# Performance work log

Hardware: AMD Instinct MI355X
Metric: run time of the kernel (lower is better)

## Reference

```python
import jax, jax.numpy as jnp
import numpy as np

INF = 1000000.0
B, S, D, N, H = 2, 2048, 1024, 16, 64
T = 2 * S
NORM = 1.0 / np.sqrt(H)


def _rel_shift(x, k_len, shift=1):
    # x: [b, n, f, t] -> Transformer-XL relative shift -> [b, n, f, k_len]
    b, n, f, t = x.shape
    y = x.reshape(b, n, t, f)[:, :, shift:, :].reshape(b, n, f, t - shift)
    return y[:, :, :, :k_len]


def setup_inputs() -> dict:
    key = jax.random.key(0)
    ks = jax.random.split(key, 16)
    inp = {}
    inp['q'] = jax.random.normal(ks[0], (B, S, D), jnp.float32)
    inp['k'] = jax.random.normal(ks[1], (B, S, D), jnp.float32)
    inp['v'] = jax.random.normal(ks[2], (B, S, D), jnp.float32)
    inp['pos_enc'] = jax.random.normal(ks[3], (T, D), jnp.float32)
    seg_ids = jax.random.randint(ks[4], (B, S), 0, 2)
    inp['seg_mat'] = seg_ids[:, :, None] == seg_ids[:, None, :]  # [B,S,S] bool
    # causal mask: 1 where attention is forbidden (j > i)
    causal = (jnp.arange(S)[None, :] > jnp.arange(S)[:, None]).astype(jnp.float32)
    inp['attn_mask'] = jnp.broadcast_to(causal[None, None], (B, 1, S, S))
    std = np.sqrt(1.0 / (D + N * H))
    inp['qW'] = jax.random.normal(ks[5], (D, N, H), jnp.float32) * std
    inp['kW'] = jax.random.normal(ks[6], (D, N, H), jnp.float32) * std
    inp['kb'] = jnp.zeros((N, H), jnp.float32)
    inp['vW'] = jax.random.normal(ks[7], (D, N, H), jnp.float32) * std
    inp['vb'] = jnp.zeros((N, H), jnp.float32)
    inp['r_w_bias'] = jax.random.uniform(ks[8], (N, H), jnp.float32, 0.0, 0.1)
    inp['r_r_bias'] = jax.random.uniform(ks[9], (N, H), jnp.float32, 0.0, 0.1)
    inp['r_kernel'] = jax.random.uniform(ks[10], (D, N, H), jnp.float32, 0.0, 0.1)
    inp['r_s_bias'] = jax.random.uniform(ks[11], (N, H), jnp.float32, 0.0, 0.1)
    inp['seg_embed'] = jax.random.uniform(ks[12], (2, N, H), jnp.float32, 0.0, 0.1)
    inp['postW'] = jax.random.normal(ks[13], (N, H, D), jnp.float32) * std
    inp['postb'] = jnp.zeros((D,), jnp.float32)
    inp['ln_g'] = jnp.ones((D,), jnp.float32)
    inp['ln_b'] = jnp.zeros((D,), jnp.float32)
    return inp


def reference(q, k, v, pos_enc, seg_mat, attn_mask, qW, kW, kb, vW, vb,
              r_w_bias, r_r_bias, r_kernel, r_s_bias, seg_embed,
              postW, postb, ln_g, ln_b):
    # head projections
    q_head = jnp.einsum('bid,dnh->binh', q, qW) * NORM
    k_head = jnp.einsum('bjd,dnh->bjnh', k, kW) + kb
    v_head = jnp.einsum('bjd,dnh->bjnh', v, vW) + vb
    # content score (r_w_bias also scaled by normalizer)
    content = jnp.einsum('binh,bjnh->bnij', q_head + r_w_bias * NORM, k_head)
    # relative position bias (rel_shift branch, shift=1)
    q_r = q_head + r_r_bias * NORM
    r_head = jnp.einsum('td,dnh->tnh', pos_enc, r_kernel)
    bd = jnp.einsum('bfnh,tnh->bnft', q_r, r_head)  # [B,N,S,T]
    pos_bias = _rel_shift(bd, S, shift=1)           # [B,N,S,S]
    # segment bias
    sb = jnp.einsum('binh,snh->bnis', q_head + r_s_bias * NORM, seg_embed)
    diff, same = sb[..., 0:1], sb[..., 1:2]         # [B,N,S,1]
    seg_bias = jnp.where(seg_mat[:, None], same, diff)  # [B,N,S,S]
    # combine, mask, softmax
    score = content + pos_bias + seg_bias
    score = score.astype(jnp.float32) - INF * attn_mask
    dist = jax.nn.softmax(score, axis=-1)
    # attention output
    attn_vec = jnp.einsum('bnij,bjnh->binh', dist, v_head)
    attn_out = jnp.einsum('binh,nhd->bid', attn_vec, postW) + postb
    # residual + layer norm
    x = q + attn_out
    mu = jnp.mean(x, axis=-1, keepdims=True)
    var = jnp.var(x, axis=-1, keepdims=True)
    return (x - mu) * jax.lax.rsqrt(var + 1e-5) * ln_g + ln_b
```

## Files before the change

kernel.cpp:

```cpp
#include <hip/hip_runtime.h>
#include <hip/hip_bf16.h>

typedef __attribute__((ext_vector_type(8))) short bf16x8;
typedef __attribute__((ext_vector_type(4))) float f32x4;
typedef unsigned short ushort_t;

#define S_LEN 2048
#define DMODEL 1024
#define NORM_F 0.125f

__device__ __forceinline__ short f2b(float x) {
  union { float f; unsigned u; } c; c.f = x;
  unsigned r = (c.u + 0x7FFFu + ((c.u >> 16) & 1u)) >> 16;
  return (short)r;
}
__device__ __forceinline__ float b2f(ushort_t u) {
  union { unsigned u; float f; } c; c.u = ((unsigned)u) << 16; return c.f;
}
__device__ __forceinline__ unsigned cvtpk(float lo, float hi) {
  unsigned r;
  asm volatile("v_cvt_pk_bf16_f32 %0, %1, %2" : "=v"(r) : "v"(lo), "v"(hi));
  return r;
}

__global__ void seg_extract_kernel(const unsigned int* __restrict__ seg_raw,
                                   unsigned* __restrict__ segw) {
  __shared__ int bad_int, bad_flt;
  int tid = threadIdx.x;
  if (tid == 0) { bad_int = 0; bad_flt = 0; }
  __syncthreads();
  for (int i = tid; i < 2048; i += 256) {
    unsigned v = seg_raw[i];
    if (v > 1u) atomicOr(&bad_int, 1);
    if (v != 0u && v != 0x3F800000u) atomicOr(&bad_flt, 1);
  }
  __syncthreads();
  int mode = bad_int ? (bad_flt ? 2 : 1) : 0;
  const unsigned char* u8 = (const unsigned char*)seg_raw;
  int P = blockIdx.x * 256 + tid;
  int b = P >> 11, i = P & 2047;
  size_t off = (size_t)b * S_LEN * S_LEN + i;
  int bit;
  if (mode == 0)      bit = (int)(seg_raw[off] & 1u);
  else if (mode == 1) bit = (seg_raw[off] != 0u) ? 1 : 0;
  else                bit = (int)(u8[off] & 1u);
  unsigned long long mk = __ballot(bit);
  if ((tid & 63) == 0) {
    segw[P >> 5] = (unsigned)mk;
    segw[(P >> 5) + 1] = (unsigned)(mk >> 32);
  }
}

__global__ __launch_bounds__(256) void conv4_kernel(
    const float* __restrict__ s0, const float* __restrict__ s1,
    const float* __restrict__ s2, const float* __restrict__ s3,
    ushort_t* __restrict__ d0, ushort_t* __restrict__ d1,
    ushort_t* __restrict__ d2, ushort_t* __restrict__ d3) {
  int z = blockIdx.y;
  const float* src = z == 0 ? s0 : z == 1 ? s1 : z == 2 ? s2 : s3;
  ushort_t* dst = z == 0 ? d0 : z == 1 ? d1 : z == 2 ? d2 : d3;
  size_t base = ((size_t)blockIdx.x * 256 + threadIdx.x) * 8;
  float4 a = *(const float4*)(src + base);
  float4 b = *(const float4*)(src + base + 4);
  union { ushort_t us[8]; uint4 v; } o;
  o.us[0] = (ushort_t)f2b(a.x); o.us[1] = (ushort_t)f2b(a.y);
  o.us[2] = (ushort_t)f2b(a.z); o.us[3] = (ushort_t)f2b(a.w);
  o.us[4] = (ushort_t)f2b(b.x); o.us[5] = (ushort_t)f2b(b.y);
  o.us[6] = (ushort_t)f2b(b.z); o.us[7] = (ushort_t)f2b(b.w);
  *(uint4*)(dst + base) = o.v;
}

__global__ __launch_bounds__(256) void convT_kernel(
    const float* __restrict__ s0, const float* __restrict__ s1,
    const float* __restrict__ s2, const float* __restrict__ s3,
    const float* __restrict__ s4,
    ushort_t* __restrict__ d0, ushort_t* __restrict__ d1,
    ushort_t* __restrict__ d2, ushort_t* __restrict__ d3,
    ushort_t* __restrict__ d4) {
  int z = blockIdx.z;
  const float* src = z == 0 ? s0 : z == 1 ? s1 : z == 2 ? s2 : z == 3 ? s3 : s4;
  ushort_t* dst = z == 0 ? d0 : z == 1 ? d1 : z == 2 ? d2 : z == 3 ? d3 : d4;
  __shared__ float Tl[64][68];
  int tid = threadIdx.x;
  int k0 = blockIdx.x * 64, n0 = blockIdx.y * 64;
#pragma unroll
  for (int it = 0; it < 4; ++it) {
    int idx = tid + it * 256;
    int r = idx >> 4, c4 = (idx & 15) * 4;
    *(float4*)&Tl[r][c4] = *(const float4*)(src + (size_t)(k0 + r) * 1024 + n0 + c4);
  }
  __syncthreads();
#pragma unroll
  for (int it = 0; it < 2; ++it) {
    int idx = tid + it * 256;
    int nn = idx >> 3, kc = idx & 7;
    union { ushort_t us[8]; uint4 v; } o;
#pragma unroll
    for (int e = 0; e < 8; ++e) o.us[e] = (ushort_t)f2b(Tl[kc * 8 + e][nn]);
    *(uint4*)(dst + (size_t)(n0 + nn) * 1024 + k0 + kc * 8) = o.v;
  }
}

template <bool OUTBF>
__global__ __launch_bounds__(256) void gemm_bf_kernel(
    const ushort_t* __restrict__ A, const ushort_t* __restrict__ Wt,
    const float* __restrict__ bias, void* __restrict__ Cv, float scale) {
  __shared__ short A_lds[128][40];
  __shared__ short B_lds[128][40];
  const int tid = threadIdx.x;
  const int wave = tid >> 6, lane = tid & 63;
  const int r16 = lane & 15, g = lane >> 4;
  const int wm = wave >> 1, wn = wave & 1;
  const int m0 = blockIdx.x * 128, n0 = blockIdx.y * 128;
  const int sr = tid >> 2, sseg = (tid & 3) * 8;
  f32x4 acc[4][4] = {};
  uint4 ra0 = *(const uint4*)(A + (size_t)(m0 + sr) * 1024 + sseg);
  uint4 ra1 = *(const uint4*)(A + (size_t)(m0 + 64 + sr) * 1024 + sseg);
  uint4 rb0 = *(const uint4*)(Wt + (size_t)(n0 + sr) * 1024 + sseg);
  uint4 rb1 = *(const uint4*)(Wt + (size_t)(n0 + 64 + sr) * 1024 + sseg);
  for (int k0 = 0; k0 < 1024; k0 += 32) {
    *(uint4*)&A_lds[sr][sseg] = ra0;
    *(uint4*)&A_lds[64 + sr][sseg] = ra1;
    *(uint4*)&B_lds[sr][sseg] = rb0;
    *(uint4*)&B_lds[64 + sr][sseg] = rb1;
    __syncthreads();
    if (k0 + 32 < 1024) {
      ra0 = *(const uint4*)(A + (size_t)(m0 + sr) * 1024 + k0 + 32 + sseg);
      ra1 = *(const uint4*)(A + (size_t)(m0 + 64 + sr) * 1024 + k0 + 32 + sseg);
      rb0 = *(const uint4*)(Wt + (size_t)(n0 + sr) * 1024 + k0 + 32 + sseg);
      rb1 = *(const uint4*)(Wt + (size_t)(n0 + 64 + sr) * 1024 + k0 + 32 + sseg);
    }
    bf16x8 af[4], bfr[4];
#pragma unroll
    for (int fm = 0; fm < 4; ++fm)
      af[fm] = *(const bf16x8*)&A_lds[wm * 64 + fm * 16 + r16][g * 8];
#pragma unroll
    for (int fn = 0; fn < 4; ++fn)
      bfr[fn] = *(const bf16x8*)&B_lds[wn * 64 + fn * 16 + r16][g * 8];
#pragma unroll
    for (int fm = 0; fm < 4; ++fm)
#pragma unroll
      for (int fn = 0; fn < 4; ++fn)
        acc[fm][fn] = __builtin_amdgcn_mfma_f32_16x16x32_bf16(af[fm], bfr[fn], acc[fm][fn], 0, 0, 0);
    __syncthreads();
  }
  float bv[4];
#pragma unroll
  for (int fn = 0; fn < 4; ++fn)
    bv[fn] = bias ? bias[n0 + wn * 64 + fn * 16 + r16] : 0.f;
#pragma unroll
  for (int fm = 0; fm < 4; ++fm)
#pragma unroll
    for (int fn = 0; fn < 4; ++fn)
#pragma unroll
      for (int rr = 0; rr < 4; ++rr) {
        float vv = acc[fm][fn][rr] * scale + bv[fn];
        size_t off = (size_t)(m0 + wm * 64 + fm * 16 + g * 4 + rr) * 1024 +
                     n0 + wn * 64 + fn * 16 + r16;
        if (OUTBF) ((ushort_t*)Cv)[off] = (ushort_t)f2b(vv);
        else       ((float*)Cv)[off] = vv;
      }
}

__global__ __launch_bounds__(256) void gemm4_kernel(
    const ushort_t* __restrict__ a0, const ushort_t* __restrict__ a1,
    const ushort_t* __restrict__ a2, const ushort_t* __restrict__ a3,
    const ushort_t* __restrict__ w0, const ushort_t* __restrict__ w1,
    const ushort_t* __restrict__ w2, const ushort_t* __restrict__ w3,
    const float* __restrict__ kb, const float* __restrict__ vb,
    ushort_t* __restrict__ c0, ushort_t* __restrict__ c1,
    ushort_t* __restrict__ c2, ushort_t* __restrict__ c3) {
  const int z = blockIdx.z;
  const ushort_t* A  = z == 0 ? a0 : z == 1 ? a1 : z == 2 ? a2 : a3;
  const ushort_t* Wt = z == 0 ? w0 : z == 1 ? w1 : z == 2 ? w2 : w3;
  const float* bias  = z == 1 ? kb : z == 2 ? vb : (const float*)nullptr;
  ushort_t* C        = z == 0 ? c0 : z == 1 ? c1 : z == 2 ? c2 : c3;
  const float scale  = z == 0 ? NORM_F : 1.0f;

  __shared__ short A_lds[128][40];
  __shared__ short B_lds[128][40];
  const int tid = threadIdx.x;
  const int wave = tid >> 6, lane = tid & 63;
  const int r16 = lane & 15, g = lane >> 4;
  const int wm = wave >> 1, wn = wave & 1;
  const int m0 = blockIdx.x * 128, n0 = blockIdx.y * 128;
  const int sr = tid >> 2, sseg = (tid & 3) * 8;
  f32x4 acc[4][4] = {};
  uint4 ra0 = *(const uint4*)(A + (size_t)(m0 + sr) * 1024 + sseg);
  uint4 ra1 = *(const uint4*)(A + (size_t)(m0 + 64 + sr) * 1024 + sseg);
  uint4 rb0 = *(const uint4*)(Wt + (size_t)(n0 + sr) * 1024 + sseg);
  uint4 rb1 = *(const uint4*)(Wt + (size_t)(n0 + 64 + sr) * 1024 + sseg);
  for (int k0 = 0; k0 < 1024; k0 += 32) {
    *(uint4*)&A_lds[sr][sseg] = ra0;
    *(uint4*)&A_lds[64 + sr][sseg] = ra1;
    *(uint4*)&B_lds[sr][sseg] = rb0;
    *(uint4*)&B_lds[64 + sr][sseg] = rb1;
    __syncthreads();
    if (k0 + 32 < 1024) {
      ra0 = *(const uint4*)(A + (size_t)(m0 + sr) * 1024 + k0 + 32 + sseg);
      ra1 = *(const uint4*)(A + (size_t)(m0 + 64 + sr) * 1024 + k0 + 32 + sseg);
      rb0 = *(const uint4*)(Wt + (size_t)(n0 + sr) * 1024 + k0 + 32 + sseg);
      rb1 = *(const uint4*)(Wt + (size_t)(n0 + 64 + sr) * 1024 + k0 + 32 + sseg);
    }
    bf16x8 af[4], bfr[4];
#pragma unroll
    for (int fm = 0; fm < 4; ++fm)
      af[fm] = *(const bf16x8*)&A_lds[wm * 64 + fm * 16 + r16][g * 8];
#pragma unroll
    for (int fn = 0; fn < 4; ++fn)
      bfr[fn] = *(const bf16x8*)&B_lds[wn * 64 + fn * 16 + r16][g * 8];
#pragma unroll
    for (int fm = 0; fm < 4; ++fm)
#pragma unroll
      for (int fn = 0; fn < 4; ++fn)
        acc[fm][fn] = __builtin_amdgcn_mfma_f32_16x16x32_bf16(af[fm], bfr[fn], acc[fm][fn], 0, 0, 0);
    __syncthreads();
  }
  float bv[4];
#pragma unroll
  for (int fn = 0; fn < 4; ++fn)
    bv[fn] = bias ? bias[n0 + wn * 64 + fn * 16 + r16] : 0.f;
#pragma unroll
  for (int fm = 0; fm < 4; ++fm)
#pragma unroll
    for (int fn = 0; fn < 4; ++fn)
#pragma unroll
      for (int rr = 0; rr < 4; ++rr) {
        float vv = acc[fm][fn][rr] * scale + bv[fn];
        size_t off = (size_t)(m0 + wm * 64 + fm * 16 + g * 4 + rr) * 1024 +
                     n0 + wn * 64 + fn * 16 + r16;
        C[off] = (ushort_t)f2b(vv);
      }
}

__global__ __launch_bounds__(256) void qprep_kernel(
    const ushort_t* __restrict__ qh, const float* __restrict__ rwb,
    const float* __restrict__ rrb, const float* __restrict__ rsb,
    const float* __restrict__ sem, ushort_t* __restrict__ qwb,
    ushort_t* __restrict__ qrb, float2* __restrict__ sbp) {
  const int tid = threadIdx.x;
  const int w = tid >> 6, lane = tid & 63;
  const int c0 = lane * 16;
  float rwbN[16], rrbN[16], rsbN[16], s0v[16], s1v[16];
#pragma unroll
  for (int u = 0; u < 16; u += 4) {
    *(float4*)&rwbN[u] = *(const float4*)(rwb + c0 + u);
    *(float4*)&rrbN[u] = *(const float4*)(rrb + c0 + u);
    *(float4*)&rsbN[u] = *(const float4*)(rsb + c0 + u);
    *(float4*)&s0v[u]  = *(const float4*)(sem + c0 + u);
    *(float4*)&s1v[u]  = *(const float4*)(sem + 1024 + c0 + u);
  }
#pragma unroll
  for (int u = 0; u < 16; ++u) { rwbN[u] *= NORM_F; rrbN[u] *= NORM_F; rsbN[u] *= NORM_F; }
  for (int r = 0; r < 16; ++r) {
    int row = blockIdx.x * 64 + w * 16 + r;
    const ushort_t* qp = qh + (size_t)row * 1024 + c0;
    union { uint4 v; ushort_t us[8]; } qa, qb;
    qa.v = *(const uint4*)qp; qb.v = *(const uint4*)(qp + 8);
    float p0 = 0.f, p1 = 0.f;
    union { ushort_t us[8]; uint4 v; } w0, w1, r0, r1;
#pragma unroll
    for (int u = 0; u < 16; ++u) {
      float qv = b2f(u < 8 ? qa.us[u] : qb.us[u - 8]);
      ushort_t cw = (ushort_t)f2b(qv + rwbN[u]);
      ushort_t cr = (ushort_t)f2b(qv + rrbN[u]);
      if (u < 8) { w0.us[u] = cw; r0.us[u] = cr; }
      else       { w1.us[u - 8] = cw; r1.us[u - 8] = cr; }
      float qs = qv + rsbN[u];
      p0 += qs * s0v[u]; p1 += qs * s1v[u];
    }
    *(uint4*)(qwb + (size_t)row * 1024 + c0)     = w0.v;
    *(uint4*)(qwb + (size_t)row * 1024 + c0 + 8) = w1.v;
    *(uint4*)(qrb + (size_t)row * 1024 + c0)     = r0.v;
    *(uint4*)(qrb + (size_t)row * 1024 + c0 + 8) = r1.v;
    p0 += __shfl_xor(p0, 1); p0 += __shfl_xor(p0, 2);
    p1 += __shfl_xor(p1, 1); p1 += __shfl_xor(p1, 2);
    if ((lane & 3) == 0) {
      int bI = row >> 11, iI = row & 2047, nI = lane >> 2;
      sbp[((size_t)bI * 16 + nI) * 2048 + iI] = make_float2(p0, p1);
    }
  }
}

__global__ __launch_bounds__(256) void attn_kernel(
    const ushort_t* __restrict__ qwb, const ushort_t* __restrict__ qrb,
    const ushort_t* __restrict__ khb, const ushort_t* __restrict__ vhb,
    const ushort_t* __restrict__ rhb, const float2* __restrict__ sbp,
    const unsigned* __restrict__ segw, ushort_t* __restrict__ opart,
    float* __restrict__ ml) {
  __shared__ short Klds[64][64];
  __shared__ short Rlds[128][64];
  __shared__ short VsT[2][64][72];
  __shared__ short SP[4][1376];

  const int tid = threadIdx.x;
  const int w = tid >> 6, lane = tid & 63;
  const int r16 = lane & 15, g = lane >> 4;
  const int lin = (int)blockIdx.x;
  const int grp = (lin & 7) + ((lin >> 9) << 3);
  const int j = (lin >> 3) & 63;
  const int x = 31 - (j >> 1);
  const int hx = j & 1;
  const int i0 = x * 64;
  const int nh = (x + 2) >> 1;
  const int tbeg = hx ? nh : 0;
  const int tend = hx ? (x + 1) : nh;
  const int n = grp & 15, b = grp >> 4;
  const int BNS = 65536;
  const int rowbase = (b * 16 + n) * 2048 + i0;

  if (tbeg >= tend) {
    const int il0 = w * 16 + g * 4;
#pragma unroll
    for (int rr = 0; rr < 4; ++rr) {
#pragma unroll
      for (int s = 0; s < 4; ++s)
        opart[(size_t)(BNS + rowbase + il0 + rr) * 64 + s * 16 + r16] = 0;
      if (r16 == 0) {
        ml[2 * BNS + rowbase + il0 + rr] = -1e30f;
        ml[3 * BNS + rowbase + il0 + rr] = 0.f;
      }
    }
    return;
  }

  short* SPw = &SP[w][0];
  const int srow = tid >> 3, sg8 = (tid & 7) * 8;

  const int qrow = i0 + w * 16 + r16;
  const ushort_t* qwp = qwb + (size_t)(b * S_LEN + qrow) * DMODEL + n * 64 + g * 8;
  const ushort_t* qrp = qrb + (size_t)(b * S_LEN + qrow) * DMODEL + n * 64 + g * 8;
  bf16x8 qw[2], qr[2];
  qw[0] = *(const bf16x8*)qwp;  qw[1] = *(const bf16x8*)(qwp + 32);
  qr[0] = *(const bf16x8*)qrp;  qr[1] = *(const bf16x8*)(qrp + 32);
  float2 sbv = sbp[((size_t)b * 16 + n) * 2048 + qrow];
  const float sb0 = sbv.x, sb1 = sbv.y;
  const int ai = (segw[b * 64 + (qrow >> 5)] >> (qrow & 31)) & 1;
  const int iw0 = i0 + w * 16;

  {
    const int j0 = tbeg * 64;
    const int W0 = 2048 + j0 - i0 - 63;
#pragma unroll
    for (int it = 0; it < 2; ++it) {
      int qk = tid + it * 256, row = qk >> 3, cl = qk & 7;
      uint4 kv = *(const uint4*)(khb + (size_t)(b * S_LEN + j0 + row) * DMODEL + n * 64 + cl * 8);
      *(uint4*)&Klds[row][(cl ^ (row & 7)) * 8] = kv;
    }
#pragma unroll
    for (int it = 0; it < 4; ++it) {
      int qk = tid + it * 256, row = qk >> 3, cl = qk & 7;
      uint4 rv = *(const uint4*)(rhb + (size_t)(W0 + row) * DMODEL + n * 64 + cl * 8);
      *(uint4*)&Rlds[row][(cl ^ (row & 7)) * 8] = rv;
    }
#pragma unroll
    for (int it = 0; it < 2; ++it) {
      int jj = srow + it * 32;
      union { uint4 v; ushort_t us[8]; } vv;
      vv.v = *(const uint4*)(vhb + (size_t)(b * S_LEN + j0 + jj) * DMODEL + n * 64 + sg8);
#pragma unroll
      for (int e = 0; e < 8; ++e) {
        int hh = sg8 + e;
        VsT[0][hh][((jj >> 3) ^ ((hh >> 3) & 3)) * 8 + (jj & 7)] = (short)vv.us[e];
      }
    }
  }

  float m_r = -1e30f, l_r = 0.f;
  f32x4 o[4] = {};

  for (int t = tbeg; t < tend; ++t) {
    const int j0 = t * 64;
    const int tt = (t - tbeg) & 1;
    const bool hasn = (t + 1 < tend);
    __syncthreads();

    uint4 kpf[2], rpf[4], vpf[2];
    if (hasn) {
      const int j0n = j0 + 64;
      const int W0n = 2048 + j0n - i0 - 63;
#pragma unroll
      for (int it = 0; it < 2; ++it) {
        int qk = tid + it * 256, row = qk >> 3, cl = qk & 7;
        kpf[it] = *(const uint4*)(khb + (size_t)(b * S_LEN + j0n + row) * DMODEL + n * 64 + cl * 8);
      }
#pragma unroll
      for (int it = 0; it < 4; ++it) {
        int qk = tid + it * 256, row = qk >> 3, cl = qk & 7;
        rpf[it] = *(const uint4*)(rhb + (size_t)(W0n + row) * DMODEL + n * 64 + cl * 8);
      }
#pragma unroll
      for (int it = 0; it < 2; ++it)
        vpf[it] = *(const uint4*)(vhb + (size_t)(b * S_LEN + j0n + srow + it * 32) * DMODEL + n * 64 + sg8);
    }
    unsigned wlo = segw[b * 64 + (j0 >> 5)];
    unsigned whi = segw[b * 64 + (j0 >> 5) + 1];

    f32x4 cf[4] = {};
#pragma unroll
    for (int s = 0; s < 4; ++s) {
      int row = s * 16 + r16;
      bf16x8 k0 = *(const bf16x8*)&Klds[row][(g ^ (row & 7)) * 8];
      bf16x8 k1 = *(const bf16x8*)&Klds[row][((4 + g) ^ (row & 7)) * 8];
      cf[s] = __builtin_amdgcn_mfma_f32_16x16x32_bf16(k0, qw[0], cf[s], 0, 0, 0);
      cf[s] = __builtin_amdgcn_mfma_f32_16x16x32_bf16(k1, qw[1], cf[s], 0, 0, 0);
    }
#pragma unroll
    for (int sp = 0; sp < 5; ++sp) {
      int row = 48 - w * 16 + sp * 16 + r16;
      bf16x8 r0 = *(const bf16x8*)&Rlds[row][(g ^ (row & 7)) * 8];
      bf16x8 r1 = *(const bf16x8*)&Rlds[row][((4 + g) ^ (row & 7)) * 8];
      f32x4 pf = {};
      pf = __builtin_amdgcn_mfma_f32_16x16x32_bf16(r0, qr[0], pf, 0, 0, 0);
      pf = __builtin_amdgcn_mfma_f32_16x16x32_bf16(r1, qr[1], pf, 0, 0, 0);
      uint2 pw;
      pw.x = cvtpk(pf[0], pf[1]);
      pw.y = cvtpk(pf[2], pf[3]);
      *(uint2*)&SPw[r16 * 84 + sp * 16 + g * 4] = pw;
    }
    ushort_t pu[4][4];
#pragma unroll
    for (int s = 0; s < 4; ++s)
#pragma unroll
      for (int rr = 0; rr < 4; ++rr)
        pu[s][rr] = (ushort_t)SPw[r16 * 84 + (15 - r16) + s * 16 + g * 4 + rr];
    float vals[4][4];
    float vmax = -1e30f;
    const bool diag = (t == x);
#pragma unroll
    for (int s = 0; s < 4; ++s) {
      unsigned word = (s < 2) ? wlo : whi;
#pragma unroll
      for (int rr = 0; rr < 4; ++rr) {
        int p = s * 16 + g * 4 + rr;
        int bitv = (word >> (p & 31)) & 1;
        float sv = cf[s][rr] + b2f(pu[s][rr]) + ((bitv == ai) ? sb1 : sb0);
        if (diag && (p > w * 16 + r16)) sv -= 1e6f;
        vals[s][rr] = sv;
        vmax = fmaxf(vmax, sv);
      }
    }
    vmax = fmaxf(vmax, __shfl_xor(vmax, 16));
    vmax = fmaxf(vmax, __shfl_xor(vmax, 32));
    float scl = 1.f;
    bool resc = !__all(vmax <= m_r + 8.f);
    if (resc) {
      float mnew = fmaxf(m_r, vmax);
      scl = __expf(m_r - mnew);
      m_r = mnew;
    }
    float pex[4][4];
    float psum = 0.f;
#pragma unroll
    for (int s = 0; s < 4; ++s)
#pragma unroll
      for (int rr = 0; rr < 4; ++rr) {
        pex[s][rr] = __expf(vals[s][rr] - m_r);
        psum += pex[s][rr];
      }
    l_r = l_r * scl + psum;
#pragma unroll
    for (int s = 0; s < 4; ++s) {
      uint2 pw;
      pw.x = cvtpk(pex[s][0], pex[s][1]);
      pw.y = cvtpk(pex[s][2], pex[s][3]);
      *(uint2*)&SPw[r16 * 72 + s * 16 + g * 4] = pw;
    }
    __syncthreads();

    if (hasn) {
#pragma unroll
      for (int it = 0; it < 2; ++it) {
        int qk = tid + it * 256, row = qk >> 3, cl = qk & 7;
        *(uint4*)&Klds[row][(cl ^ (row & 7)) * 8] = kpf[it];
      }
#pragma unroll
      for (int it = 0; it < 4; ++it) {
        int qk = tid + it * 256, row = qk >> 3, cl = qk & 7;
        *(uint4*)&Rlds[row][(cl ^ (row & 7)) * 8] = rpf[it];
      }
      const int dst = tt ^ 1;
#pragma unroll
      for (int it = 0; it < 2; ++it) {
        int jj = srow + it * 32;
        union { uint4 v; ushort_t us[8]; } vv; vv.v = vpf[it];
#pragma unroll
        for (int e = 0; e < 8; ++e) {
          int hh = sg8 + e;
          VsT[dst][hh][((jj >> 3) ^ ((hh >> 3) & 3)) * 8 + (jj & 7)] = (short)vv.us[e];
        }
      }
    }
    if (resc) {
      float sclb[4];
#pragma unroll
      for (int rr = 0; rr < 4; ++rr) sclb[rr] = __shfl(scl, g * 4 + rr);
#pragma unroll
      for (int s = 0; s < 4; ++s)
#pragma unroll
        for (int rr = 0; rr < 4; ++rr) o[s][rr] *= sclb[rr];
    }
    bf16x8 pa0 = *(const bf16x8*)&SPw[r16 * 72 + g * 8];
    bf16x8 pa1 = *(const bf16x8*)&SPw[r16 * 72 + 32 + g * 8];
#pragma unroll
    for (int s = 0; s < 4; ++s) {
      int hh = s * 16 + r16;
      bf16x8 v0 = *(const bf16x8*)&VsT[tt][hh][(g ^ ((hh >> 3) & 3)) * 8];
      bf16x8 v1 = *(const bf16x8*)&VsT[tt][hh][((4 + g) ^ ((hh >> 3) & 3)) * 8];
      o[s] = __builtin_amdgcn_mfma_f32_16x16x32_bf16(pa0, v0, o[s], 0, 0, 0);
      o[s] = __builtin_amdgcn_mfma_f32_16x16x32_bf16(pa1, v1, o[s], 0, 0, 0);
    }
  }

  float l_row = l_r;
  l_row += __shfl_xor(l_row, 16);
  l_row += __shfl_xor(l_row, 32);
  if (lane < 16) {
    ml[hx * 2 * BNS + rowbase + w * 16 + r16] = m_r;
    ml[(hx * 2 + 1) * BNS + rowbase + w * 16 + r16] = l_row;
  }
#pragma unroll
  for (int s = 0; s < 4; ++s)
#pragma unroll
    for (int rr = 0; rr < 4; ++rr) {
      const int il = w * 16 + g * 4 + rr;
      opart[(size_t)(hx * BNS + rowbase + il) * 64 + s * 16 + r16] = (ushort_t)f2b(o[s][rr]);
    }
}

__global__ __launch_bounds__(256) void merge_kernel(
    const ushort_t* __restrict__ opart, const float* __restrict__ ml,
    ushort_t* __restrict__ av) {
  const int BNS = 65536;
  int row = blockIdx.x * 4 + (threadIdx.x >> 6);
  int lane = threadIdx.x & 63;
  float m0 = ml[row], l0 = ml[BNS + row];
  float m1 = ml[2 * BNS + row], l1 = ml[3 * BNS + row];
  float m = fmaxf(m0, m1);
  float a0 = __expf(m0 - m), a1 = __expf(m1 - m);
  float inv = 1.f / (l0 * a0 + l1 * a1);
  float o0 = b2f(opart[(size_t)row * 64 + lane]);
  float o1 = b2f(opart[(size_t)(BNS + row) * 64 + lane]);
  float ov = (o0 * a0 + o1 * a1) * inv;
  int bI = row >> 15, nI = (row >> 11) & 15, iI = row & 2047;
  av[(size_t)(bI * 2048 + iI) * 1024 + nI * 64 + lane] = (ushort_t)f2b(ov);
}

__global__ __launch_bounds__(256) void ln_kernel(
    const float* __restrict__ q, const float* __restrict__ ao,
    const float* __restrict__ ln_g, const float* __restrict__ ln_b,
    float* __restrict__ out) {
  int row = blockIdx.x;
  const float* xq = q + (size_t)row * 1024;
  const float* xa = ao + (size_t)row * 1024;
  float x[4], lsum = 0.f, lsq = 0.f;
#pragma unroll
  for (int e = 0; e < 4; ++e) {
    int d = threadIdx.x + e * 256;
    x[e] = xq[d] + xa[d];
    lsum += x[e]; lsq += x[e] * x[e];
  }
  for (int off = 1; off < 64; off <<= 1) {
    lsum += __shfl_xor(lsum, off);
    lsq += __shfl_xor(lsq, off);
  }
  __shared__ float red[8];
  int wv = threadIdx.x >> 6, ln = threadIdx.x & 63;
  if (ln == 0) { red[wv] = lsum; red[4 + wv] = lsq; }
  __syncthreads();
  lsum = red[0] + red[1] + red[2] + red[3];
  lsq = red[4] + red[5] + red[6] + red[7];
  float mu = lsum * (1.f / 1024.f);
  float var = lsq * (1.f / 1024.f) - mu * mu;
  float inv = rsqrtf(var + 1e-5f);
#pragma unroll
  for (int e = 0; e < 4; ++e) {
    int d = threadIdx.x + e * 256;
    out[(size_t)row * 1024 + d] = (x[e] - mu) * inv * ln_g[d] + ln_b[d];
  }
}

extern "C" void kernel_launch(void* const* d_in, const int* in_sizes, int n_in,
                              void* d_out, int out_size, void* d_ws, size_t ws_size,
                              hipStream_t stream) {
  const float* q   = (const float*)d_in[0];
  const float* k   = (const float*)d_in[1];
  const float* v   = (const float*)d_in[2];
  const float* pe  = (const float*)d_in[3];
  const void*  seg = d_in[4];
  const float* qW  = (const float*)d_in[6];
  const float* kW  = (const float*)d_in[7];
  const float* kb  = (const float*)d_in[8];
  const float* vW  = (const float*)d_in[9];
  const float* vb  = (const float*)d_in[10];
  const float* rwb = (const float*)d_in[11];
  const float* rrb = (const float*)d_in[12];
  const float* rK  = (const float*)d_in[13];
  const float* rsb = (const float*)d_in[14];
  const float* sem = (const float*)d_in[15];
  const float* pW  = (const float*)d_in[16];
  const float* pb  = (const float*)d_in[17];
  const float* lng = (const float*)d_in[18];
  const float* lnb = (const float*)d_in[19];
  float* out = (float*)d_out;

  const size_t MB = 1u << 20;
  char* W = (char*)d_ws;
  ushort_t* abq  = (ushort_t*)(W + 0 * MB);
  ushort_t* abk  = (ushort_t*)(W + 8 * MB);
  ushort_t* abv  = (ushort_t*)(W + 16 * MB);
  ushort_t* abpe = (ushort_t*)(W + 24 * MB);
  ushort_t* wtq  = (ushort_t*)(W + 32 * MB);
  ushort_t* wtk  = (ushort_t*)(W + 34 * MB);
  ushort_t* wtv  = (ushort_t*)(W + 36 * MB);
  ushort_t* wtr  = (ushort_t*)(W + 38 * MB);
  ushort_t* wtp  = (ushort_t*)(W + 40 * MB);
  ushort_t* qh   = (ushort_t*)(W + 42 * MB);
  ushort_t* kh   = (ushort_t*)(W + 50 * MB);
  ushort_t* vh   = (ushort_t*)(W + 58 * MB);
  ushort_t* rh   = (ushort_t*)(W + 66 * MB);
  unsigned* segw = (unsigned*)(W + 74 * MB);
  float2*   sbp  = (float2*)(W + 74 * MB + 65536);
  float*    ml   = (float*)(W + 75 * MB);
  ushort_t* qwb   = (ushort_t*)(W + 0 * MB);
  ushort_t* qrb   = (ushort_t*)(W + 8 * MB);
  ushort_t* opart = (ushort_t*)(W + 16 * MB);
  ushort_t* av    = (ushort_t*)(W + 42 * MB);
  float*    ao    = (float*)(W + 50 * MB);

  seg_extract_kernel<<<dim3(16), dim3(256), 0, stream>>>((const unsigned int*)seg, segw);
  conv4_kernel<<<dim3(2048, 4), dim3(256), 0, stream>>>(q, k, v, pe, abq, abk, abv, abpe);
  convT_kernel<<<dim3(16, 16, 5), dim3(256), 0, stream>>>(qW, kW, vW, rK, pW,
                                                          wtq, wtk, wtv, wtr, wtp);
  gemm4_kernel<<<dim3(32, 8, 4), dim3(256), 0, stream>>>(
      abq, abk, abv, abpe, wtq, wtk, wtv, wtr, kb, vb, qh, kh, vh, rh);

  qprep_kernel<<<dim3(64), dim3(256), 0, stream>>>(qh, rwb, rrb, rsb, sem, qwb, qrb, sbp);

  attn_kernel<<<dim3(2048), dim3(256), 0, stream>>>(qwb, qrb, kh, vh, rh,
                                                    sbp, segw, opart, ml);
  merge_kernel<<<dim3(16384), dim3(256), 0, stream>>>(opart, ml, av);

  gemm_bf_kernel<false><<<dim3(32, 8), dim3(256), 0, stream>>>(av, wtp, pb, ao, 1.0f);
  ln_kernel<<<dim3(4096), dim3(256), 0, stream>>>(q, ao, lng, lnb, out);
}
```

Before: 283.2 us.

## Retile post GEMM, split qprep blocks, widen V swizzle, add MFMA priority hints

The output projection GEMM now uses 64-row tiles, launching twice as many blocks to fill more CUs. qprep runs as 256 single-wave blocks instead of 64 four-wave blocks. The V-transpose LDS swizzle XORs the full hh>>3 to spread bank accesses more widely. s_setprio hints around the score and PV MFMA sections favour matrix issue across waves. Smaller tiles lower per-block data reuse, and the priority hints may do little.

```diff
diff --git a/kernel.cpp b/kernel.cpp
--- a/kernel.cpp
+++ b/kernel.cpp
@@ -101,10 +101,21 @@
   }
 }
 
-template <bool OUTBF>
-__global__ __launch_bounds__(256) void gemm_bf_kernel(
-    const ushort_t* __restrict__ A, const ushort_t* __restrict__ Wt,
-    const float* __restrict__ bias, void* __restrict__ Cv, float scale) {
+__global__ __launch_bounds__(256) void gemm4_kernel(
+    const ushort_t* __restrict__ a0, const ushort_t* __restrict__ a1,
+    const ushort_t* __restrict__ a2, const ushort_t* __restrict__ a3,
+    const ushort_t* __restrict__ w0, const ushort_t* __restrict__ w1,
+    const ushort_t* __restrict__ w2, const ushort_t* __restrict__ w3,
+    const float* __restrict__ kb, const float* __restrict__ vb,
+    ushort_t* __restrict__ c0, ushort_t* __restrict__ c1,
+    ushort_t* __restrict__ c2, ushort_t* __restrict__ c3) {
+  const int z = blockIdx.z;
+  const ushort_t* A  = z == 0 ? a0 : z == 1 ? a1 : z == 2 ? a2 : a3;
+  const ushort_t* Wt = z == 0 ? w0 : z == 1 ? w1 : z == 2 ? w2 : w3;
+  const float* bias  = z == 1 ? kb : z == 2 ? vb : (const float*)nullptr;
+  ushort_t* C        = z == 0 ? c0 : z == 1 ? c1 : z == 2 ? c2 : c3;
+  const float scale  = z == 0 ? NORM_F : 1.0f;
+
   __shared__ short A_lds[128][40];
   __shared__ short B_lds[128][40];
   const int tid = threadIdx.x;
@@ -157,60 +168,44 @@
         float vv = acc[fm][fn][rr] * scale + bv[fn];
         size_t off = (size_t)(m0 + wm * 64 + fm * 16 + g * 4 + rr) * 1024 +
                      n0 + wn * 64 + fn * 16 + r16;
-        if (OUTBF) ((ushort_t*)Cv)[off] = (ushort_t)f2b(vv);
-        else       ((float*)Cv)[off] = vv;
-      }
-}
-
-__global__ __launch_bounds__(256) void gemm4_kernel(
-    const ushort_t* __restrict__ a0, const ushort_t* __restrict__ a1,
-    const ushort_t* __restrict__ a2, const ushort_t* __restrict__ a3,
-    const ushort_t* __restrict__ w0, const ushort_t* __restrict__ w1,
-    const ushort_t* __restrict__ w2, const ushort_t* __restrict__ w3,
-    const float* __restrict__ kb, const float* __restrict__ vb,
-    ushort_t* __restrict__ c0, ushort_t* __restrict__ c1,
-    ushort_t* __restrict__ c2, ushort_t* __restrict__ c3) {
-  const int z = blockIdx.z;
-  const ushort_t* A  = z == 0 ? a0 : z == 1 ? a1 : z == 2 ? a2 : a3;
-  const ushort_t* Wt = z == 0 ? w0 : z == 1 ? w1 : z == 2 ? w2 : w3;
-  const float* bias  = z == 1 ? kb : z == 2 ? vb : (const float*)nullptr;
-  ushort_t* C        = z == 0 ? c0 : z == 1 ? c1 : z == 2 ? c2 : c3;
-  const float scale  = z == 0 ? NORM_F : 1.0f;
-
-  __shared__ short A_lds[128][40];
+        C[off] = (ushort_t)f2b(vv);
+      }
+}
+
+__global__ __launch_bounds__(256) void gemm_post_kernel(
+    const ushort_t* __restrict__ A, const ushort_t* __restrict__ Wt,
+    const float* __restrict__ bias, float* __restrict__ C) {
+  __shared__ short A_lds[64][40];
   __shared__ short B_lds[128][40];
   const int tid = threadIdx.x;
   const int wave = tid >> 6, lane = tid & 63;
   const int r16 = lane & 15, g = lane >> 4;
   const int wm = wave >> 1, wn = wave & 1;
-  const int m0 = blockIdx.x * 128, n0 = blockIdx.y * 128;
+  const int m0 = blockIdx.x * 64, n0 = blockIdx.y * 128;
   const int sr = tid >> 2, sseg = (tid & 3) * 8;
-  f32x4 acc[4][4] = {};
+  f32x4 acc[2][4] = {};
   uint4 ra0 = *(const uint4*)(A + (size_t)(m0 + sr) * 1024 + sseg);
-  uint4 ra1 = *(const uint4*)(A + (size_t)(m0 + 64 + sr) * 1024 + sseg);
   uint4 rb0 = *(const uint4*)(Wt + (size_t)(n0 + sr) * 1024 + sseg);
   uint4 rb1 = *(const uint4*)(Wt + (size_t)(n0 + 64 + sr) * 1024 + sseg);
   for (int k0 = 0; k0 < 1024; k0 += 32) {
     *(uint4*)&A_lds[sr][sseg] = ra0;
-    *(uint4*)&A_lds[64 + sr][sseg] = ra1;
     *(uint4*)&B_lds[sr][sseg] = rb0;
     *(uint4*)&B_lds[64 + sr][sseg] = rb1;
     __syncthreads();
     if (k0 + 32 < 1024) {
       ra0 = *(const uint4*)(A + (size_t)(m0 + sr) * 1024 + k0 + 32 + sseg);
-      ra1 = *(const uint4*)(A + (size_t)(m0 + 64 + sr) * 1024 + k0 + 32 + sseg);
       rb0 = *(const uint4*)(Wt + (size_t)(n0 + sr) * 1024 + k0 + 32 + sseg);
       rb1 = *(const uint4*)(Wt + (size_t)(n0 + 64 + sr) * 1024 + k0 + 32 + sseg);
     }
-    bf16x8 af[4], bfr[4];
-#pragma unroll
-    for (int fm = 0; fm < 4; ++fm)
-      af[fm] = *(const bf16x8*)&A_lds[wm * 64 + fm * 16 + r16][g * 8];
+    bf16x8 af[2], bfr[4];
+#pragma unroll
+    for (int fm = 0; fm < 2; ++fm)
+      af[fm] = *(const bf16x8*)&A_lds[wm * 32 + fm * 16 + r16][g * 8];
 #pragma unroll
     for (int fn = 0; fn < 4; ++fn)
       bfr[fn] = *(const bf16x8*)&B_lds[wn * 64 + fn * 16 + r16][g * 8];
 #pragma unroll
-    for (int fm = 0; fm < 4; ++fm)
+    for (int fm = 0; fm < 2; ++fm)
 #pragma unroll
       for (int fn = 0; fn < 4; ++fn)
         acc[fm][fn] = __builtin_amdgcn_mfma_f32_16x16x32_bf16(af[fm], bfr[fn], acc[fm][fn], 0, 0, 0);
@@ -221,25 +216,23 @@
   for (int fn = 0; fn < 4; ++fn)
     bv[fn] = bias ? bias[n0 + wn * 64 + fn * 16 + r16] : 0.f;
 #pragma unroll
-  for (int fm = 0; fm < 4; ++fm)
+  for (int fm = 0; fm < 2; ++fm)
 #pragma unroll
     for (int fn = 0; fn < 4; ++fn)
 #pragma unroll
       for (int rr = 0; rr < 4; ++rr) {
-        float vv = acc[fm][fn][rr] * scale + bv[fn];
-        size_t off = (size_t)(m0 + wm * 64 + fm * 16 + g * 4 + rr) * 1024 +
+        size_t off = (size_t)(m0 + wm * 32 + fm * 16 + g * 4 + rr) * 1024 +
                      n0 + wn * 64 + fn * 16 + r16;
-        C[off] = (ushort_t)f2b(vv);
-      }
-}
-
-__global__ __launch_bounds__(256) void qprep_kernel(
+        C[off] = acc[fm][fn][rr] + bv[fn];
+      }
+}
+
+__global__ __launch_bounds__(64) void qprep_kernel(
     const ushort_t* __restrict__ qh, const float* __restrict__ rwb,
     const float* __restrict__ rrb, const float* __restrict__ rsb,
     const float* __restrict__ sem, ushort_t* __restrict__ qwb,
     ushort_t* __restrict__ qrb, float2* __restrict__ sbp) {
-  const int tid = threadIdx.x;
-  const int w = tid >> 6, lane = tid & 63;
+  const int lane = threadIdx.x & 63;
   const int c0 = lane * 16;
   float rwbN[16], rrbN[16], rsbN[16], s0v[16], s1v[16];
 #pragma unroll
@@ -253,7 +246,7 @@
 #pragma unroll
   for (int u = 0; u < 16; ++u) { rwbN[u] *= NORM_F; rrbN[u] *= NORM_F; rsbN[u] *= NORM_F; }
   for (int r = 0; r < 16; ++r) {
-    int row = blockIdx.x * 64 + w * 16 + r;
+    int row = blockIdx.x * 16 + r;
     const ushort_t* qp = qh + (size_t)row * 1024 + c0;
     union { uint4 v; ushort_t us[8]; } qa, qb;
     qa.v = *(const uint4*)qp; qb.v = *(const uint4*)(qp + 8);
@@ -361,7 +354,7 @@
 #pragma unroll
       for (int e = 0; e < 8; ++e) {
         int hh = sg8 + e;
-        VsT[0][hh][((jj >> 3) ^ ((hh >> 3) & 3)) * 8 + (jj & 7)] = (short)vv.us[e];
+        VsT[0][hh][((jj >> 3) ^ (hh >> 3)) * 8 + (jj & 7)] = (short)vv.us[e];
       }
     }
   }
@@ -396,6 +389,7 @@
     unsigned wlo = segw[b * 64 + (j0 >> 5)];
     unsigned whi = segw[b * 64 + (j0 >> 5) + 1];
 
+    __builtin_amdgcn_s_setprio(1);
     f32x4 cf[4] = {};
 #pragma unroll
     for (int s = 0; s < 4; ++s) {
@@ -418,6 +412,7 @@
       pw.y = cvtpk(pf[2], pf[3]);
       *(uint2*)&SPw[r16 * 84 + sp * 16 + g * 4] = pw;
     }
+    __builtin_amdgcn_s_setprio(0);
     ushort_t pu[4][4];
 #pragma unroll
     for (int s = 0; s < 4; ++s)
@@ -487,7 +482,7 @@
 #pragma unroll
         for (int e = 0; e < 8; ++e) {
           int hh = sg8 + e;
-          VsT[dst][hh][((jj >> 3) ^ ((hh >> 3) & 3)) * 8 + (jj & 7)] = (short)vv.us[e];
+          VsT[dst][hh][((jj >> 3) ^ (hh >> 3)) * 8 + (jj & 7)] = (short)vv.us[e];
         }
       }
     }
@@ -502,14 +497,16 @@
     }
     bf16x8 pa0 = *(const bf16x8*)&SPw[r16 * 72 + g * 8];
     bf16x8 pa1 = *(const bf16x8*)&SPw[r16 * 72 + 32 + g * 8];
+    __builtin_amdgcn_s_setprio(1);
 #pragma unroll
     for (int s = 0; s < 4; ++s) {
       int hh = s * 16 + r16;
-      bf16x8 v0 = *(const bf16x8*)&VsT[tt][hh][(g ^ ((hh >> 3) & 3)) * 8];
-      bf16x8 v1 = *(const bf16x8*)&VsT[tt][hh][((4 + g) ^ ((hh >> 3) & 3)) * 8];
+      bf16x8 v0 = *(const bf16x8*)&VsT[tt][hh][(g ^ (hh >> 3)) * 8];
+      bf16x8 v1 = *(const bf16x8*)&VsT[tt][hh][((4 + g) ^ (hh >> 3)) * 8];
       o[s] = __builtin_amdgcn_mfma_f32_16x16x32_bf16(pa0, v0, o[s], 0, 0, 0);
       o[s] = __builtin_amdgcn_mfma_f32_16x16x32_bf16(pa1, v1, o[s], 0, 0, 0);
     }
+    __builtin_amdgcn_s_setprio(0);
   }
 
   float l_row = l_r;
@@ -635,12 +632,12 @@
   gemm4_kernel<<<dim3(32, 8, 4), dim3(256), 0, stream>>>(
       abq, abk, abv, abpe, wtq, wtk, wtv, wtr, kb, vb, qh, kh, vh, rh);
 
-  qprep_kernel<<<dim3(64), dim3(256), 0, stream>>>(qh, rwb, rrb, rsb, sem, qwb, qrb, sbp);
+  qprep_kernel<<<dim3(256), dim3(64), 0, stream>>>(qh, rwb, rrb, rsb, sem, qwb, qrb, sbp);
 
   attn_kernel<<<dim3(2048), dim3(256), 0, stream>>>(qwb, qrb, kh, vh, rh,
                                                     sbp, segw, opart, ml);
   merge_kernel<<<dim3(16384), dim3(256), 0, stream>>>(opart, ml, av);
 
-  gemm_bf_kernel<false><<<dim3(32, 8), dim3(256), 0, stream>>>(av, wtp, pb, ao, 1.0f);
+  gemm_post_kernel<<<dim3(64, 8), dim3(256), 0, stream>>>(av, wtp, pb, ao);
   ln_kernel<<<dim3(4096), dim3(256), 0, stream>>>(q, ao, lng, lnb, out);
 }
```

Result: faster. 274.6 us (-3.0%).
